# Kernel optimization log

Measured on AMD Instinct MI355X. Metric: run time of the kernel, lower is better.

## Reference

```python
import jax, jax.numpy as jnp
import numpy as np

BETA = 0.5
TEMPERATURE = 1.0
IGNORE_INDEX = -100
BT, H, V = 2048, 2048, 32000


def setup_inputs() -> dict:
    key = jax.random.key(0)
    k1, k2, k3, k4, k5 = jax.random.split(key, 5)
    return {
        "student_input": jax.random.normal(k1, (BT, H), dtype=jnp.float32),
        "student_weight": jax.random.normal(k2, (V, H), dtype=jnp.float32) * 0.02,
        "teacher_input": jax.random.normal(k3, (BT, H), dtype=jnp.float32),
        "teacher_weight": jax.random.normal(k4, (V, H), dtype=jnp.float32) * 0.02,
        "labels": jax.random.randint(k5, (BT,), 0, V, dtype=jnp.int64),
    }


def reference(student_input, student_weight, teacher_input, teacher_weight, labels):
    # logits = x @ W^T, scaled by temperature, then log-softmax (computed in fp32)
    s_logits = jnp.einsum("bh,vh->bv", student_input, student_weight).astype(jnp.float32)
    t_logits = jnp.einsum("bh,vh->bv", teacher_input, teacher_weight).astype(jnp.float32)
    s_lp = jax.nn.log_softmax(s_logits / TEMPERATURE, axis=-1)  # log Q, (BT, V)
    t_lp = jax.nn.log_softmax(t_logits / TEMPERATURE, axis=-1)  # log P, (BT, V)
    Q = jnp.exp(s_lp)
    P = jnp.exp(t_lp)
    # generalized JSD: M = beta*P + (1-beta)*Q
    log_m = jnp.log(BETA * P + (1.0 - BETA) * Q)
    per_row = jnp.sum(BETA * P * (t_lp - log_m) + (1.0 - BETA) * Q * (s_lp - log_m), axis=-1)  # (BT,)
    valid = (labels != IGNORE_INDEX)
    n_non_ignore = jnp.maximum(jnp.sum(valid), 1).astype(jnp.float32)
    loss = jnp.sum(jnp.where(valid, per_row, 0.0)) / n_non_ignore
    return loss
```

## Files before the change

kernel.cpp:

```cpp
#include <hip/hip_runtime.h>
#include <stdint.h>

#define BT 2048
#define H  2048
#define V  32000

typedef __attribute__((ext_vector_type(8))) short short8;
typedef __attribute__((ext_vector_type(4))) float f32x4;

__device__ inline unsigned short f2bf(float x) {
  unsigned int u = __float_as_uint(x);
  u += 0x7FFFu + ((u >> 16) & 1u);
  return (unsigned short)(u >> 16);
}

__global__ void zero_accum(float* accum) {
  accum[0] = 0.0f;
  ((unsigned int*)accum)[1] = 0u;
}

__global__ __launch_bounds__(256) void cvt_kernel(const float* __restrict__ src,
                                                  unsigned short* __restrict__ dst,
                                                  int n8) {
  int i = blockIdx.x * blockDim.x + threadIdx.x;
  if (i >= n8) return;
  const float4* s = (const float4*)src;
  float4 a = s[2 * i];
  float4 b = s[2 * i + 1];
  union { unsigned short us[8]; uint4 v; } o;
  o.us[0] = f2bf(a.x); o.us[1] = f2bf(a.y); o.us[2] = f2bf(a.z); o.us[3] = f2bf(a.w);
  o.us[4] = f2bf(b.x); o.us[5] = f2bf(b.y); o.us[6] = f2bf(b.z); o.us[7] = f2bf(b.w);
  ((uint4*)dst)[i] = o.v;
}

#define GBM 256
#define GBN 256
#define GBK 32
#define NKT (H / GBK)


#define GLL(gp, lp) __builtin_amdgcn_global_load_lds( \
    (const __attribute__((address_space(1))) unsigned int*)(gp), \
    (__attribute__((address_space(3))) unsigned int*)(lp), 16, 0, 0)

__global__ __launch_bounds__(512, 2) void gemm_bt(const unsigned short* __restrict__ A0,
                                                  const unsigned short* __restrict__ B0,
                                                  const unsigned short* __restrict__ A1,
                                                  const unsigned short* __restrict__ B1,
                                                  unsigned short* __restrict__ C0,
                                                  unsigned short* __restrict__ C1) {
  const int z = blockIdx.z;
  const unsigned short* Amat = z ? A1 : A0;
  const unsigned short* Bmat = z ? B1 : B0;
  unsigned short* C = z ? C1 : C0;

  const int m0 = blockIdx.x * GBM;
  const int n0 = blockIdx.y * GBN;

  __shared__ alignas(16) unsigned short lA[4][8192];
  __shared__ alignas(16) unsigned short lB[4][8192];

  const int tid  = threadIdx.x;
  const int lane = tid & 63;
  const int w    = tid >> 6;
  const int wm   = w >> 2;
  const int wn   = w & 3;
  const int l4   = lane & 15;
  const int q    = lane >> 4;

  const unsigned short* ga[2];
  const unsigned short* gb[2];
  #pragma unroll
  for (int j = 0; j < 2; j++) {
    int p   = tid + j * 512;
    int pr  = p >> 3;
    int s0  = (p & 7) ^ ((pr & 3) << 1);
    int row = (pr << 1) | (s0 & 1);
    int cc  = s0 >> 1;
    ga[j] = Amat + (size_t)(m0 + row) * H + cc * 8;
    gb[j] = Bmat + (size_t)(n0 + row) * H + cc * 8;
  }

  const int s0f   = ((q << 1) | (l4 & 1)) ^ (l4 & 6);
  const int Abase = (wm * 64 + (l4 >> 1)) * 64 + s0f * 8;
  const int Bbase = (wn * 32 + (l4 >> 1)) * 64 + s0f * 8;

  f32x4 acc[8][4];
  #pragma unroll
  for (int i = 0; i < 8; i++)
    #pragma unroll
    for (int j = 0; j < 4; j++)
      acc[i][j] = (f32x4){0.f, 0.f, 0.f, 0.f};

  #pragma unroll
  for (int t = 0; t < 3; t++) {
    GLL(ga[0] + t * GBK, &lA[t][w * 512]);
    GLL(ga[1] + t * GBK, &lA[t][w * 512 + 4096]);
    GLL(gb[0] + t * GBK, &lB[t][w * 512]);
    GLL(gb[1] + t * GBK, &lB[t][w * 512 + 4096]);
  }
  asm volatile("s_waitcnt vmcnt(8)" ::: "memory");
  __builtin_amdgcn_s_barrier();

  for (int t = 0; t < NKT; ++t) {
    const int cur = t & 3;
    const bool st = (t + 3) < NKT;
    const int  sb = (t + 3) & 3;

    short8 af[4], bf[4];
    #pragma unroll
    for (int mf = 0; mf < 4; mf++) af[mf] = *(const short8*)&lA[cur][Abase + mf * 512];
    #pragma unroll
    for (int nf = 0; nf < 4; nf++) bf[nf] = *(const short8*)&lB[cur][Bbase + nf * 512];
    if (st) {
      GLL(ga[0] + (t + 3) * GBK, &lA[sb][w * 512]);
      GLL(ga[1] + (t + 3) * GBK, &lA[sb][w * 512 + 4096]);
    }
    __builtin_amdgcn_s_barrier();
    asm volatile("s_waitcnt lgkmcnt(0)" ::: "memory");
    __builtin_amdgcn_s_setprio(1);
    #pragma unroll
    for (int mf = 0; mf < 4; mf++)
      #pragma unroll
      for (int nf = 0; nf < 4; nf++)
        acc[mf][nf] = __builtin_amdgcn_mfma_f32_16x16x32_bf16(af[mf], bf[nf], acc[mf][nf], 0, 0, 0);
    __builtin_amdgcn_s_setprio(0);
    __builtin_amdgcn_s_barrier();

    short8 ag[4];
    #pragma unroll
    for (int mf = 0; mf < 4; mf++) ag[mf] = *(const short8*)&lA[cur][Abase + (mf + 4) * 512];
    if (st) {
      GLL(gb[0] + (t + 3) * GBK, &lB[sb][w * 512]);
      GLL(gb[1] + (t + 3) * GBK, &lB[sb][w * 512 + 4096]);
    }
    __builtin_amdgcn_s_barrier();
    asm volatile("s_waitcnt lgkmcnt(0)" ::: "memory");
    __builtin_amdgcn_s_setprio(1);
    #pragma unroll
    for (int mf = 0; mf < 4; mf++)
      #pragma unroll
      for (int nf = 0; nf < 4; nf++)
        acc[mf + 4][nf] = __builtin_amdgcn_mfma_f32_16x16x32_bf16(ag[mf], bf[nf], acc[mf + 4][nf], 0, 0, 0);
    __builtin_amdgcn_s_setprio(0);

    if (t < NKT - 3)       asm volatile("s_waitcnt vmcnt(8)" ::: "memory");
    else if (t == NKT - 3) asm volatile("s_waitcnt vmcnt(4)" ::: "memory");
    else                   asm volatile("s_waitcnt vmcnt(0)" ::: "memory");
    __builtin_amdgcn_s_barrier();
  }

  #pragma unroll
  for (int mf = 0; mf < 8; mf++)
    #pragma unroll
    for (int nf = 0; nf < 4; nf++)
      #pragma unroll
      for (int r = 0; r < 4; r++) {
        int gr = m0 + wm * 128 + mf * 16 + q * 4 + r;
        int gc = n0 + wn * 64 + nf * 16 + l4;
        C[(size_t)gr * V + gc] = f2bf(acc[mf][nf][r]);
      }
}

__device__ inline void unpack8(uint4 v, float* f) {
  f[0] = __uint_as_float(v.x << 16);
  f[1] = __uint_as_float(v.x & 0xFFFF0000u);
  f[2] = __uint_as_float(v.y << 16);
  f[3] = __uint_as_float(v.y & 0xFFFF0000u);
  f[4] = __uint_as_float(v.z << 16);
  f[5] = __uint_as_float(v.z & 0xFFFF0000u);
  f[6] = __uint_as_float(v.w << 16);
  f[7] = __uint_as_float(v.w & 0xFFFF0000u);
}

__device__ inline float blk_max(float v, float* red, int tid) {
  #pragma unroll
  for (int o = 32; o > 0; o >>= 1) v = fmaxf(v, __shfl_xor(v, o, 64));
  __syncthreads();
  if ((tid & 63) == 0) red[tid >> 6] = v;
  __syncthreads();
  return fmaxf(fmaxf(red[0], red[1]), fmaxf(red[2], red[3]));
}

__device__ inline float blk_sum(float v, float* red, int tid) {
  #pragma unroll
  for (int o = 32; o > 0; o >>= 1) v += __shfl_xor(v, o, 64);
  __syncthreads();
  if ((tid & 63) == 0) red[tid >> 6] = v;
  __syncthreads();
  return (red[0] + red[1]) + (red[2] + red[3]);
}

__global__ __launch_bounds__(256) void jsd_kernel(const unsigned short* __restrict__ Slog,
                                                  const unsigned short* __restrict__ Tlog,
                                                  const long long* __restrict__ labels,
                                                  float* __restrict__ accum) {
  const int r   = blockIdx.x;
  const int tid = threadIdx.x;
  __shared__ float red[4];

  const uint4* s4 = (const uint4*)(Slog + (size_t)r * V);
  const uint4* t4 = (const uint4*)(Tlog + (size_t)r * V);
  const int NC = V / 8;

  float sm = -1e30f, ss = 0.f, tm = -1e30f, ts = 0.f;
  for (int c = tid; c < NC; c += 256) {
    uint4 sv = s4[c], tv = t4[c];
    float fs[8], ft[8];
    unpack8(sv, fs); unpack8(tv, ft);
    float lms = fs[0], lmt = ft[0];
    #pragma unroll
    for (int j = 1; j < 8; j++) { lms = fmaxf(lms, fs[j]); lmt = fmaxf(lmt, ft[j]); }
    if (lms > sm) { ss *= __expf(sm - lms); sm = lms; }
    if (lmt > tm) { ts *= __expf(tm - lmt); tm = lmt; }
    #pragma unroll
    for (int j = 0; j < 8; j++) {
      ss += __expf(fs[j] - sm);
      ts += __expf(ft[j] - tm);
    }
  }
  float SM = blk_max(sm, red, tid);
  ss *= __expf(sm - SM);
  float SS = blk_sum(ss, red, tid);
  float TM = blk_max(tm, red, tid);
  ts *= __expf(tm - TM);
  float TS = blk_sum(ts, red, tid);
  float slse = SM + __logf(SS);
  float tlse = TM + __logf(TS);

  float loss = 0.f;
  for (int c = tid; c < NC; c += 256) {
    uint4 sv = s4[c], tv = t4[c];
    float fs[8], ft[8];
    unpack8(sv, fs); unpack8(tv, ft);
    #pragma unroll
    for (int j = 0; j < 8; j++) {
      float sl = fs[j] - slse;
      float tl = ft[j] - tlse;
      float qv = __expf(sl);
      float pv = __expf(tl);
      float m  = 0.5f * (pv + qv);
      float lm = __logf(m);
      loss += 0.5f * (pv * (tl - lm) + qv * (sl - lm));
    }
  }
  loss = blk_sum(loss, red, tid);

  if (tid == 0) {
    long long lab = labels[r];
    if (lab != -100LL) {
      atomicAdd(&accum[0], loss);
      atomicAdd((unsigned int*)&accum[1], 1u);
    }
  }
}

__global__ void finalize(const float* __restrict__ accum, float* __restrict__ out) {
  float cnt = (float)((const unsigned int*)accum)[1];
  out[0] = accum[0] / fmaxf(cnt, 1.0f);
}

extern "C" void kernel_launch(void* const* d_in, const int* in_sizes, int n_in,
                              void* d_out, int out_size, void* d_ws, size_t ws_size,
                              hipStream_t stream) {
  const float* s_in = (const float*)d_in[0];
  const float* s_w  = (const float*)d_in[1];
  const float* t_in = (const float*)d_in[2];
  const float* t_w  = (const float*)d_in[3];
  const long long* labels = (const long long*)d_in[4];
  float* out = (float*)d_out;

  char* ws = (char*)d_ws;
  size_t off = 0;
  auto take = [&](size_t bytes) -> char* {
    char* p = ws + off;
    off += (bytes + 255) & ~(size_t)255;
    return p;
  };
  unsigned short* sw_bf = (unsigned short*)take((size_t)V * H * 2);
  unsigned short* tw_bf = (unsigned short*)take((size_t)V * H * 2);
  unsigned short* si_bf = (unsigned short*)take((size_t)BT * H * 2);
  unsigned short* ti_bf = (unsigned short*)take((size_t)BT * H * 2);
  unsigned short* slog  = (unsigned short*)take((size_t)BT * V * 2);
  unsigned short* tlog  = (unsigned short*)take((size_t)BT * V * 2);
  float* accum = (float*)take(256);
  if (off > ws_size) return;

  zero_accum<<<dim3(1), dim3(1), 0, stream>>>(accum);

  const int nW8 = (V * H) / 8;
  const int nI8 = (BT * H) / 8;
  cvt_kernel<<<dim3((nW8 + 255) / 256), dim3(256), 0, stream>>>(s_w, sw_bf, nW8);
  cvt_kernel<<<dim3((nW8 + 255) / 256), dim3(256), 0, stream>>>(t_w, tw_bf, nW8);
  cvt_kernel<<<dim3((nI8 + 255) / 256), dim3(256), 0, stream>>>(s_in, si_bf, nI8);
  cvt_kernel<<<dim3((nI8 + 255) / 256), dim3(256), 0, stream>>>(t_in, ti_bf, nI8);

  gemm_bt<<<dim3(BT / GBM, V / GBN, 2), dim3(512), 0, stream>>>(si_bf, sw_bf, ti_bf, tw_bf, slog, tlog);

  jsd_kernel<<<dim3(BT), dim3(256), 0, stream>>>(slog, tlog, labels, accum);

  finalize<<<dim3(1), dim3(1), 0, stream>>>(accum, out);
}
```

Baseline: 1.271 ms.

## Software-pipeline LDS fragment loads across K tiles with double-buffered registers

```diff
diff --git a/kernel.cpp b/kernel.cpp
--- a/kernel.cpp
+++ b/kernel.cpp
@@ -101,54 +101,71 @@
   }
   asm volatile("s_waitcnt vmcnt(8)" ::: "memory");
   __builtin_amdgcn_s_barrier();
-
-  for (int t = 0; t < NKT; ++t) {
-    const int cur = t & 3;
-    const bool st = (t + 3) < NKT;
-    const int  sb = (t + 3) & 3;
-
-    short8 af[4], bf[4];
-    #pragma unroll
-    for (int mf = 0; mf < 4; mf++) af[mf] = *(const short8*)&lA[cur][Abase + mf * 512];
-    #pragma unroll
-    for (int nf = 0; nf < 4; nf++) bf[nf] = *(const short8*)&lB[cur][Bbase + nf * 512];
-    if (st) {
-      GLL(ga[0] + (t + 3) * GBK, &lA[sb][w * 512]);
-      GLL(ga[1] + (t + 3) * GBK, &lA[sb][w * 512 + 4096]);
-    }
-    __builtin_amdgcn_s_barrier();
-    asm volatile("s_waitcnt lgkmcnt(0)" ::: "memory");
-    __builtin_amdgcn_s_setprio(1);
-    #pragma unroll
-    for (int mf = 0; mf < 4; mf++)
-      #pragma unroll
-      for (int nf = 0; nf < 4; nf++)
-        acc[mf][nf] = __builtin_amdgcn_mfma_f32_16x16x32_bf16(af[mf], bf[nf], acc[mf][nf], 0, 0, 0);
-    __builtin_amdgcn_s_setprio(0);
-    __builtin_amdgcn_s_barrier();
-
-    short8 ag[4];
-    #pragma unroll
-    for (int mf = 0; mf < 4; mf++) ag[mf] = *(const short8*)&lA[cur][Abase + (mf + 4) * 512];
-    if (st) {
-      GLL(gb[0] + (t + 3) * GBK, &lB[sb][w * 512]);
-      GLL(gb[1] + (t + 3) * GBK, &lB[sb][w * 512 + 4096]);
-    }
-    __builtin_amdgcn_s_barrier();
-    asm volatile("s_waitcnt lgkmcnt(0)" ::: "memory");
-    __builtin_amdgcn_s_setprio(1);
-    #pragma unroll
-    for (int mf = 0; mf < 4; mf++)
-      #pragma unroll
-      for (int nf = 0; nf < 4; nf++)
-        acc[mf + 4][nf] = __builtin_amdgcn_mfma_f32_16x16x32_bf16(ag[mf], bf[nf], acc[mf + 4][nf], 0, 0, 0);
-    __builtin_amdgcn_s_setprio(0);
-
-    if (t < NKT - 3)       asm volatile("s_waitcnt vmcnt(8)" ::: "memory");
-    else if (t == NKT - 3) asm volatile("s_waitcnt vmcnt(4)" ::: "memory");
-    else                   asm volatile("s_waitcnt vmcnt(0)" ::: "memory");
-    __builtin_amdgcn_s_barrier();
-  }
+  asm volatile("" ::: "memory");
+
+  short8 af0[4], bf0[4], af1[4], bf1[4], ag[4];
+  #pragma unroll
+  for (int i = 0; i < 4; i++) af0[i] = *(const short8*)&lA[0][Abase + i * 512];
+  #pragma unroll
+  for (int i = 0; i < 4; i++) bf0[i] = *(const short8*)&lB[0][Bbase + i * 512];
+
+#define TILE_STEP(T, afc, bfc, afn, bfn)                                          \
+  {                                                                               \
+    const int cur_ = (T) & 3;                                                     \
+    const int sb_  = ((T) + 3) & 3;                                               \
+    const bool st_ = ((T) + 3) < NKT;                                             \
+    \
+    if (st_) {                                                                    \
+      GLL(ga[0] + ((T) + 3) * GBK, &lA[sb_][w * 512]);                            \
+      GLL(ga[1] + ((T) + 3) * GBK, &lA[sb_][w * 512 + 4096]);                     \
+    }                                                                             \
+    _Pragma("unroll")                                                             \
+    for (int i = 0; i < 4; i++) ag[i] = *(const short8*)&lA[cur_][Abase + (i + 4) * 512]; \
+    asm volatile("s_waitcnt lgkmcnt(4)" ::: "memory");  \
+    __builtin_amdgcn_sched_barrier(0);                                            \
+    __builtin_amdgcn_s_setprio(1);                                                \
+    _Pragma("unroll")                                                             \
+    for (int mf = 0; mf < 4; mf++)                                                \
+      _Pragma("unroll")                                                           \
+      for (int nf = 0; nf < 4; nf++)                                              \
+        acc[mf][nf] = __builtin_amdgcn_mfma_f32_16x16x32_bf16(afc[mf], bfc[nf], acc[mf][nf], 0, 0, 0); \
+    __builtin_amdgcn_s_setprio(0);                                                \
+    \
+    if (st_) {                                                                    \
+      GLL(gb[0] + ((T) + 3) * GBK, &lB[sb_][w * 512]);                            \
+      GLL(gb[1] + ((T) + 3) * GBK, &lB[sb_][w * 512 + 4096]);                     \
+    }                                                                             \
+    if ((T) < NKT - 3)       asm volatile("s_waitcnt vmcnt(8)" ::: "memory");     \
+    else if ((T) == NKT - 3) asm volatile("s_waitcnt vmcnt(4)" ::: "memory");     \
+    else if ((T) == NKT - 2) asm volatile("s_waitcnt vmcnt(0)" ::: "memory");     \
+    __builtin_amdgcn_s_barrier();                                                 \
+    asm volatile("" ::: "memory");                                                \
+    if ((T) + 1 < NKT) {                                                          \
+      const int nx_ = ((T) + 1) & 3;                                              \
+      _Pragma("unroll")                                                           \
+      for (int i = 0; i < 4; i++) afn[i] = *(const short8*)&lA[nx_][Abase + i * 512]; \
+      _Pragma("unroll")                                                           \
+      for (int i = 0; i < 4; i++) bfn[i] = *(const short8*)&lB[nx_][Bbase + i * 512]; \
+      asm volatile("s_waitcnt lgkmcnt(8)" ::: "memory");  \
+    } else {                                                                      \
+      asm volatile("s_waitcnt lgkmcnt(0)" ::: "memory");                          \
+    }                                                                             \
+    __builtin_amdgcn_sched_barrier(0);                                            \
+    __builtin_amdgcn_s_setprio(1);                                                \
+    _Pragma("unroll")                                                             \
+    for (int mf = 0; mf < 4; mf++)                                                \
+      _Pragma("unroll")                                                           \
+      for (int nf = 0; nf < 4; nf++)                                              \
+        acc[mf + 4][nf] = __builtin_amdgcn_mfma_f32_16x16x32_bf16(ag[mf], bfc[nf], acc[mf + 4][nf], 0, 0, 0); \
+    __builtin_amdgcn_s_setprio(0);                                                \
+    __builtin_amdgcn_s_barrier();  \
+  }
+
+  for (int t = 0; t < NKT; t += 2) {
+    TILE_STEP(t,     af0, bf0, af1, bf1);
+    TILE_STEP(t + 1, af1, bf1, af0, bf0);
+  }
+#undef TILE_STEP
 
   #pragma unroll
   for (int mf = 0; mf < 8; mf++)
```

New measurement: 1.310 ms. 1.03x slower.
